# Performance work log

Hardware: AMD Instinct MI355X
Metric: run time of the kernel (lower is better)

Reference implementation:

```python
import jax, jax.numpy as jnp
import numpy as np

EMBED = 128   # embed_dim
HEADS = 8
POINTS = 4
H_SP, W_SP = 51, 102   # hardcoded spatial_shapes in __init__
BEV = 100              # bev_res
HRES = 50              # height_res


def _make_ref_points():
    """Exact numpy replica of the spherical grid built in __init__."""
    eps = 1e-6
    x = np.linspace(-71 / 2, 71 / 2, BEV)
    y = np.linspace(-71 / 2, 71 / 2, BEV)
    z = np.linspace(-50 / 2, 50 / 2, HRES)
    gx, gy, gz = np.meshgrid(x, y, z, indexing='ij')
    phi = np.sign(gy + eps) * np.arccos(gx / (np.sqrt(gx ** 2 + gy ** 2) + eps))
    theta = np.arccos(gz / (np.sqrt(gx ** 2 + gy ** 2 + gz ** 2) + eps))
    phi = 2 * np.pi - phi
    phi[phi > 2 * np.pi] -= 2 * np.pi
    col = phi / (2 * np.pi)   # grd_col_cross
    row = theta / np.pi       # grd_row_cross
    ref = np.stack([col, row], axis=-1)              # (BEV, BEV, HRES, 2)
    ref = ref.transpose(2, 0, 1, 3).reshape(HRES, BEV * BEV, 2)
    return jnp.asarray(ref, dtype=jnp.float32)


def setup_inputs() -> dict:
    key = jax.random.key(0)
    ks = jax.random.split(key, 12)
    d = EMBED
    s = 0.02
    return {
        'query': jax.random.normal(ks[0], (1, BEV * BEV, d), jnp.float32),
        'value': jax.random.normal(ks[1], (1, H_SP * W_SP, d), jnp.float32),
        'ref_points': _make_ref_points(),
        'W_off': jax.random.normal(ks[2], (d, HEADS * POINTS * 2), jnp.float32) * s,
        'b_off': jax.random.normal(ks[3], (HEADS * POINTS * 2,), jnp.float32) * s,
        'W_attn': jax.random.normal(ks[4], (d, HEADS * POINTS), jnp.float32) * s,
        'b_attn': jax.random.normal(ks[5], (HEADS * POINTS,), jnp.float32) * s,
        'W_val': jax.random.normal(ks[6], (d, d), jnp.float32) * s,
        'b_val': jax.random.normal(ks[7], (d,), jnp.float32) * s,
        'W_out': jax.random.normal(ks[8], (d, d), jnp.float32) * s,
        'b_out': jax.random.normal(ks[9], (d,), jnp.float32) * s,
        'W_proj': jax.random.normal(ks[10], (d, 1), jnp.float32) * s,
        'b_proj': jax.random.normal(ks[11], (1,), jnp.float32) * s,
    }


def _bilinear_sample(vflat, loc):
    """grid_sample(bilinear, zero padding, align_corners=False).
    vflat: (B, H*W, hd) value maps; loc: (B, N, 2) normalized [0,1] (x,y)."""
    px = loc[..., 0] * W_SP - 0.5
    py = loc[..., 1] * H_SP - 0.5
    x0 = jnp.floor(px)
    y0 = jnp.floor(py)
    dx = (px - x0)[..., None]
    dy = (py - y0)[..., None]
    x0i = x0.astype(jnp.int32)
    y0i = y0.astype(jnp.int32)

    def gather(xi, yi):
        valid = (xi >= 0) & (xi < W_SP) & (yi >= 0) & (yi < H_SP)
        idx = jnp.clip(yi, 0, H_SP - 1) * W_SP + jnp.clip(xi, 0, W_SP - 1)
        v = jnp.take_along_axis(vflat, idx[..., None], axis=1)  # (B, N, hd)
        return v * valid[..., None].astype(vflat.dtype)

    v00 = gather(x0i, y0i)
    v01 = gather(x0i + 1, y0i)
    v10 = gather(x0i, y0i + 1)
    v11 = gather(x0i + 1, y0i + 1)
    return (v00 * (1 - dx) * (1 - dy) + v01 * dx * (1 - dy)
            + v10 * (1 - dx) * dy + v11 * dx * dy)


def reference(query, value, ref_points, W_off, b_off, W_attn, b_attn,
              W_val, b_val, W_out, b_out, W_proj, b_proj):
    bs, nq, d = query.shape
    hd = d // HEADS
    L = ref_points.shape[0]

    # query-dependent MSDA projections (identical across height levels)
    offsets = (query @ W_off + b_off).reshape(bs, nq, HEADS, POINTS, 2)
    aw = jax.nn.softmax((query @ W_attn + b_attn).reshape(bs, nq, HEADS, POINTS), axis=-1)
    awt = aw.transpose(0, 2, 1, 3)                              # (bs, heads, nq, points)
    v = (value @ W_val + b_val).reshape(bs, -1, HEADS, hd)
    vflat = v.transpose(0, 2, 1, 3).reshape(bs * HEADS, H_SP * W_SP, hd)
    norm = jnp.asarray([W_SP, H_SP], dtype=query.dtype)         # offset_normalizer [W, H]

    def per_level(ref):  # ref: (nq, 2) -> MSDA output with its internal residual
        loc = ref[None, :, None, None, :] + offsets / norm      # (bs, nq, heads, pts, 2)
        loc = loc.transpose(0, 2, 1, 3, 4).reshape(bs * HEADS, nq * POINTS, 2)
        samp = _bilinear_sample(vflat, loc).reshape(bs, HEADS, nq, POINTS, hd)
        out = jnp.einsum('bhnp,bhnpd->bnhd', awt, samp).reshape(bs, nq, d)
        return out @ W_out + b_out + query                      # mmcv MSDA adds identity

    grd = jax.vmap(per_level)(ref_points)                       # (L, bs, nq, d)
    grd_3d = grd.transpose(1, 2, 0, 3).reshape(bs, BEV, BEV, L, d)
    weights = jax.nn.softmax(grd_3d @ W_proj + b_proj, axis=3)  # (bs, BEV, BEV, L, 1)
    max_height_index = jnp.argmax(weights, axis=3)              # (bs, BEV, BEV, 1)
    grd_bev = (weights * grd_3d).sum(axis=3)                    # (bs, BEV, BEV, d)
    return grd_bev.reshape(bs, nq, d) + query, max_height_index
```

## Files before the change

### kernel.cpp

```cpp
#include <hip/hip_runtime.h>
#include <math.h>

#define EMBED   128
#define NHEADS  8
#define NPOINTS 4
#define HD      16
#define HSP     51
#define WSP     102
#define NPIX    (HSP * WSP)
#define NQ      10000
#define NLVL    50

__global__ __launch_bounds__(128) void k_prep(
    const float* __restrict__ value,
    const float* __restrict__ Wv,
    const float* __restrict__ bv,
    const float* __restrict__ query,
    const float* __restrict__ Woff,
    const float* __restrict__ boff,
    const float* __restrict__ Wattn,
    const float* __restrict__ battn,
    const float* __restrict__ Wout,
    const float* __restrict__ Wproj,
    float* __restrict__ vout,
    float* __restrict__ off_out,
    float* __restrict__ aw_out,
    float* __restrict__ u_out) {
    const int b = blockIdx.x;
    const int t = threadIdx.x;

    if (b < NPIX) {
        __shared__ float vrow[EMBED];
        vrow[t] = value[(size_t)b * EMBED + t];
        __syncthreads();
        float acc = bv[t];
#pragma unroll 8
        for (int k = 0; k < EMBED; ++k)
            acc = fmaf(vrow[k], Wv[(size_t)k * EMBED + t], acc);
        const int h = t >> 4, c = t & 15;
        vout[((size_t)h * NPIX + b) * HD + c] = acc;
    } else if (b < NPIX + NQ) {
        const int q = b - NPIX;
        __shared__ float qrow[EMBED];
        __shared__ float attn[32];
        qrow[t] = query[(size_t)q * EMBED + t];
        __syncthreads();
        if (t < 64) {
            float acc = boff[t];
#pragma unroll 8
            for (int k = 0; k < EMBED; ++k)
                acc = fmaf(qrow[k], Woff[(size_t)k * 64 + t], acc);
            off_out[(size_t)q * 64 + t] = acc;
        } else if (t < 96) {
            const int j = t - 64;
            float acc = battn[j];
#pragma unroll 8
            for (int k = 0; k < EMBED; ++k)
                acc = fmaf(qrow[k], Wattn[(size_t)k * 32 + j], acc);
            attn[j] = acc;
        }
        __syncthreads();
        if (t < NHEADS) {
            const float a0 = attn[t * 4 + 0], a1 = attn[t * 4 + 1];
            const float a2 = attn[t * 4 + 2], a3 = attn[t * 4 + 3];
            const float mx = fmaxf(fmaxf(a0, a1), fmaxf(a2, a3));
            const float e0 = __expf(a0 - mx), e1 = __expf(a1 - mx);
            const float e2 = __expf(a2 - mx), e3 = __expf(a3 - mx);
            const float inv = 1.f / (e0 + e1 + e2 + e3);
            aw_out[(size_t)q * 32 + t * 4 + 0] = e0 * inv;
            aw_out[(size_t)q * 32 + t * 4 + 1] = e1 * inv;
            aw_out[(size_t)q * 32 + t * 4 + 2] = e2 * inv;
            aw_out[(size_t)q * 32 + t * 4 + 3] = e3 * inv;
        }
    } else {
        float acc = 0.f;
#pragma unroll 8
        for (int d = 0; d < EMBED; ++d)
            acc = fmaf(Wout[(size_t)t * EMBED + d], Wproj[d], acc);
        u_out[t] = acc;
    }
}

__global__ __launch_bounds__(256) void k_main(
    const float* __restrict__ query,
    const float* __restrict__ refp,
    const float* __restrict__ voff,
    const float* __restrict__ vaw,
    const float* __restrict__ vflat,
    const float* __restrict__ uvec,
    const float* __restrict__ Wout,
    const float* __restrict__ bout,
    float* __restrict__ out0,
    float* __restrict__ out1) {
    const int t = threadIdx.x;
    const int slot = t >> 6;
    const int lane = t & 63;
    const int half = lane >> 5;
    const int sub  = lane & 31;
    const int h  = sub >> 2;
    const int c4 = sub & 3;
    const int q = blockIdx.x * 4 + slot;

    __shared__ float s_rpy[4][NLVL];
    __shared__ float4 s_lds[4][32];

    {
        int i = t;
        if (i < 4 * NLVL) {
            const int ql = i / NLVL, l = i - ql * NLVL;
            const int qq = blockIdx.x * 4 + ql;
            s_rpy[ql][l] = refp[((size_t)l * NQ + qq) * 2 + 1];
        }
    }

    const float4* offp = (const float4*)(voff + (size_t)q * 64 + h * 8);
    const float4 o01 = offp[0];
    const float4 o23 = offp[1];
    const float4 awv4 = *(const float4*)(vaw + (size_t)q * 32 + h * 4);
    const float4 u4 = *(const float4*)(uvec + h * 16 + c4 * 4);
    const float rpx = refp[(size_t)q * 2];
    const float4* vbase = (const float4*)vflat + (size_t)h * NPIX * 4 + c4;

    const float offx[4] = {o01.x, o01.z, o23.x, o23.z};
    const float offy[4] = {o01.y, o01.w, o23.y, o23.w};
    const float awv[4]  = {awv4.x, awv4.y, awv4.z, awv4.w};

    float wx0[NPOINTS], wx1[NPOINTS], oyc[NPOINTS];
    int xo0[NPOINTS], xo1[NPOINTS];
#pragma unroll
    for (int p = 0; p < NPOINTS; ++p) {
        const float px = fmaf(rpx, (float)WSP, offx[p]) - 0.5f;
        const float fx = floorf(px);
        const float dx = px - fx;
        const int x0 = (int)fx, x1 = x0 + 1;
        const float a = awv[p];
        wx0[p] = ((unsigned)x0 < (unsigned)WSP) ? a * (1.f - dx) : 0.f;
        wx1[p] = ((unsigned)x1 < (unsigned)WSP) ? a * dx : 0.f;
        xo0[p] = min(max(x0, 0), WSP - 1) * 4;
        xo1[p] = min(max(x1, 0), WSP - 1) * 4;
        oyc[p] = offy[p] - 0.5f;
    }

    __syncthreads();

    float4 acc = {0.f, 0.f, 0.f, 0.f};
    float Z = 0.f, m = -1e30f;
    int best = 0;

#pragma unroll 2
    for (int i = 0; i < NLVL / 2; ++i) {
        const int l = 2 * i + half;
        const float rpy = s_rpy[slot][l];
        float4 s = {0.f, 0.f, 0.f, 0.f};
#pragma unroll
        for (int p = 0; p < NPOINTS; ++p) {
            const float py = fmaf(rpy, (float)HSP, oyc[p]);
            const float fy = floorf(py);
            const float dy = py - fy;
            const int y0 = (int)fy, y1 = y0 + 1;
            const float t0 = ((unsigned)y0 < (unsigned)HSP) ? (1.f - dy) : 0.f;
            const float t1 = ((unsigned)y1 < (unsigned)HSP) ? dy : 0.f;
            const int rb0 = min(max(y0, 0), HSP - 1) * (WSP * 4);
            const int rb1 = min(max(y1, 0), HSP - 1) * (WSP * 4);
            const float w00 = wx0[p] * t0;
            const float w01 = wx1[p] * t0;
            const float w10 = wx0[p] * t1;
            const float w11 = wx1[p] * t1;
            const float4 v00 = vbase[rb0 + xo0[p]];
            const float4 v01 = vbase[rb0 + xo1[p]];
            const float4 v10 = vbase[rb1 + xo0[p]];
            const float4 v11 = vbase[rb1 + xo1[p]];
            s.x = fmaf(w00, v00.x, s.x); s.y = fmaf(w00, v00.y, s.y);
            s.z = fmaf(w00, v00.z, s.z); s.w = fmaf(w00, v00.w, s.w);
            s.x = fmaf(w01, v01.x, s.x); s.y = fmaf(w01, v01.y, s.y);
            s.z = fmaf(w01, v01.z, s.z); s.w = fmaf(w01, v01.w, s.w);
            s.x = fmaf(w10, v10.x, s.x); s.y = fmaf(w10, v10.y, s.y);
            s.z = fmaf(w10, v10.z, s.z); s.w = fmaf(w10, v10.w, s.w);
            s.x = fmaf(w11, v11.x, s.x); s.y = fmaf(w11, v11.y, s.y);
            s.z = fmaf(w11, v11.z, s.z); s.w = fmaf(w11, v11.w, s.w);
        }
        float part = s.x * u4.x;
        part = fmaf(s.y, u4.y, part);
        part = fmaf(s.z, u4.z, part);
        part = fmaf(s.w, u4.w, part);
#pragma unroll
        for (int d = 1; d < 32; d <<= 1)
            part += __shfl_xor(part, d, 64);
        const float e = __expf(part);
        Z += e;
        acc.x = fmaf(e, s.x, acc.x);
        acc.y = fmaf(e, s.y, acc.y);
        acc.z = fmaf(e, s.z, acc.z);
        acc.w = fmaf(e, s.w, acc.w);
        best = (part > m) ? l : best;
        m = fmaxf(part, m);
    }

    {
        const float mo = __shfl_xor(m, 32, 64);
        const int   bo = __shfl_xor(best, 32, 64);
        const float Zo = __shfl_xor(Z, 32, 64);
        const float ax = __shfl_xor(acc.x, 32, 64);
        const float ay = __shfl_xor(acc.y, 32, 64);
        const float az = __shfl_xor(acc.z, 32, 64);
        const float aw_ = __shfl_xor(acc.w, 32, 64);
        const bool takeOther = (mo > m) || (mo == m && bo < best);
        best = takeOther ? bo : best;
        Z += Zo;
        acc.x += ax; acc.y += ay; acc.z += az; acc.w += aw_;
    }
    const float inv = 1.f / Z;
    if (half == 0) {
        float4 sv;
        sv.x = acc.x * inv; sv.y = acc.y * inv;
        sv.z = acc.z * inv; sv.w = acc.w * inv;
        s_lds[slot][sub] = sv;
        if (sub == 0) out1[q] = (float)best;
    }
    __syncthreads();

    const int dpb = sub * 4;
    float4 r = {0.f, 0.f, 0.f, 0.f};
    if (half == 0) {
        const float4 b4 = *(const float4*)(bout + dpb);
        const float4 q4 = *(const float4*)(query + (size_t)q * EMBED + dpb);
        r.x = fmaf(2.f, q4.x, b4.x);
        r.y = fmaf(2.f, q4.y, b4.y);
        r.z = fmaf(2.f, q4.z, b4.z);
        r.w = fmaf(2.f, q4.w, b4.w);
    }
    const float4* srow = s_lds[slot];
    const int cg0 = half * 16;
#pragma unroll 4
    for (int cg = cg0; cg < cg0 + 16; ++cg) {
        const float4 s4 = srow[cg];
        const float4 w0 = *(const float4*)(Wout + (size_t)(cg * 4 + 0) * EMBED + dpb);
        const float4 w1 = *(const float4*)(Wout + (size_t)(cg * 4 + 1) * EMBED + dpb);
        const float4 w2 = *(const float4*)(Wout + (size_t)(cg * 4 + 2) * EMBED + dpb);
        const float4 w3 = *(const float4*)(Wout + (size_t)(cg * 4 + 3) * EMBED + dpb);
        r.x = fmaf(s4.x, w0.x, r.x); r.y = fmaf(s4.x, w0.y, r.y);
        r.z = fmaf(s4.x, w0.z, r.z); r.w = fmaf(s4.x, w0.w, r.w);
        r.x = fmaf(s4.y, w1.x, r.x); r.y = fmaf(s4.y, w1.y, r.y);
        r.z = fmaf(s4.y, w1.z, r.z); r.w = fmaf(s4.y, w1.w, r.w);
        r.x = fmaf(s4.z, w2.x, r.x); r.y = fmaf(s4.z, w2.y, r.y);
        r.z = fmaf(s4.z, w2.z, r.z); r.w = fmaf(s4.z, w2.w, r.w);
        r.x = fmaf(s4.w, w3.x, r.x); r.y = fmaf(s4.w, w3.y, r.y);
        r.z = fmaf(s4.w, w3.z, r.z); r.w = fmaf(s4.w, w3.w, r.w);
    }
    {
        const float rx = __shfl_xor(r.x, 32, 64);
        const float ry = __shfl_xor(r.y, 32, 64);
        const float rz = __shfl_xor(r.z, 32, 64);
        const float rw = __shfl_xor(r.w, 32, 64);
        r.x += rx; r.y += ry; r.z += rz; r.w += rw;
    }
    if (half == 0)
        *(float4*)(out0 + (size_t)q * EMBED + dpb) = r;
}

extern "C" void kernel_launch(void* const* d_in, const int* in_sizes, int n_in,
                              void* d_out, int out_size, void* d_ws, size_t ws_size,
                              hipStream_t stream) {
    const float* query = (const float*)d_in[0];
    const float* value = (const float*)d_in[1];
    const float* refp  = (const float*)d_in[2];
    const float* Woff  = (const float*)d_in[3];
    const float* boff  = (const float*)d_in[4];
    const float* Wattn = (const float*)d_in[5];
    const float* battn = (const float*)d_in[6];
    const float* Wval  = (const float*)d_in[7];
    const float* bval  = (const float*)d_in[8];
    const float* Wout  = (const float*)d_in[9];
    const float* bout  = (const float*)d_in[10];
    const float* Wproj = (const float*)d_in[11];

    float* ws = (float*)d_ws;
    float* ws_v   = ws;
    float* ws_off = ws_v + (size_t)NHEADS * NPIX * HD;
    float* ws_aw  = ws_off + (size_t)NQ * 64;
    float* ws_u   = ws_aw + (size_t)NQ * 32;

    float* out0 = (float*)d_out;
    float* out1 = out0 + (size_t)NQ * EMBED;

    hipLaunchKernelGGL(k_prep, dim3(NPIX + NQ + 1), dim3(128), 0, stream,
                       value, Wval, bval, query, Woff, boff, Wattn, battn,
                       Wout, Wproj, ws_v, ws_off, ws_aw, ws_u);
    hipLaunchKernelGGL(k_main, dim3(NQ / 4), dim3(256), 0, stream,
                       query, refp, ws_off, ws_aw, ws_v, ws_u, Wout, bout,
                       out0, out1);
}
```

Baseline: 253.6 us.

## Split level loop across two waves per query and pack two rows per prep block

```diff
diff --git a/kernel.cpp b/kernel.cpp
--- a/kernel.cpp
+++ b/kernel.cpp
@@ -11,7 +11,10 @@
 #define NQ      10000
 #define NLVL    50
 
-__global__ __launch_bounds__(128) void k_prep(
+#define NPB_A ((NPIX + 1) / 2)
+#define NPB_B (NQ / 2)
+
+__global__ __launch_bounds__(256) void k_prep(
     const float* __restrict__ value,
     const float* __restrict__ Wv,
     const float* __restrict__ bv,
@@ -28,60 +31,67 @@
     float* __restrict__ u_out) {
     const int b = blockIdx.x;
     const int t = threadIdx.x;
-
-    if (b < NPIX) {
-        __shared__ float vrow[EMBED];
-        vrow[t] = value[(size_t)b * EMBED + t];
+    const int unit = t >> 7;
+    const int tt = t & 127;
+
+    if (b < NPB_A) {
+        __shared__ float vrow[2][EMBED];
+        const int pix = b * 2 + unit;
+        vrow[unit][tt] = value[(size_t)pix * EMBED + tt];
         __syncthreads();
-        float acc = bv[t];
+        float acc = bv[tt];
+        const float* vr = vrow[unit];
 #pragma unroll 8
         for (int k = 0; k < EMBED; ++k)
-            acc = fmaf(vrow[k], Wv[(size_t)k * EMBED + t], acc);
-        const int h = t >> 4, c = t & 15;
-        vout[((size_t)h * NPIX + b) * HD + c] = acc;
-    } else if (b < NPIX + NQ) {
-        const int q = b - NPIX;
-        __shared__ float qrow[EMBED];
-        __shared__ float attn[32];
-        qrow[t] = query[(size_t)q * EMBED + t];
+            acc = fmaf(vr[k], Wv[(size_t)k * EMBED + tt], acc);
+        const int h = tt >> 4, c = tt & 15;
+        vout[((size_t)h * NPIX + pix) * HD + c] = acc;
+    } else if (b < NPB_A + NPB_B) {
+        const int q = (b - NPB_A) * 2 + unit;
+        __shared__ float qrow[2][EMBED];
+        __shared__ float attn[2][32];
+        qrow[unit][tt] = query[(size_t)q * EMBED + tt];
         __syncthreads();
-        if (t < 64) {
-            float acc = boff[t];
+        const float* qr = qrow[unit];
+        if (tt < 64) {
+            float acc = boff[tt];
 #pragma unroll 8
             for (int k = 0; k < EMBED; ++k)
-                acc = fmaf(qrow[k], Woff[(size_t)k * 64 + t], acc);
-            off_out[(size_t)q * 64 + t] = acc;
-        } else if (t < 96) {
-            const int j = t - 64;
+                acc = fmaf(qr[k], Woff[(size_t)k * 64 + tt], acc);
+            off_out[(size_t)q * 64 + tt] = acc;
+        } else if (tt < 96) {
+            const int j = tt - 64;
             float acc = battn[j];
 #pragma unroll 8
             for (int k = 0; k < EMBED; ++k)
-                acc = fmaf(qrow[k], Wattn[(size_t)k * 32 + j], acc);
-            attn[j] = acc;
+                acc = fmaf(qr[k], Wattn[(size_t)k * 32 + j], acc);
+            attn[unit][j] = acc;
         }
         __syncthreads();
-        if (t < NHEADS) {
-            const float a0 = attn[t * 4 + 0], a1 = attn[t * 4 + 1];
-            const float a2 = attn[t * 4 + 2], a3 = attn[t * 4 + 3];
+        if (tt < NHEADS) {
+            const float a0 = attn[unit][tt * 4 + 0], a1 = attn[unit][tt * 4 + 1];
+            const float a2 = attn[unit][tt * 4 + 2], a3 = attn[unit][tt * 4 + 3];
             const float mx = fmaxf(fmaxf(a0, a1), fmaxf(a2, a3));
             const float e0 = __expf(a0 - mx), e1 = __expf(a1 - mx);
             const float e2 = __expf(a2 - mx), e3 = __expf(a3 - mx);
             const float inv = 1.f / (e0 + e1 + e2 + e3);
-            aw_out[(size_t)q * 32 + t * 4 + 0] = e0 * inv;
-            aw_out[(size_t)q * 32 + t * 4 + 1] = e1 * inv;
-            aw_out[(size_t)q * 32 + t * 4 + 2] = e2 * inv;
-            aw_out[(size_t)q * 32 + t * 4 + 3] = e3 * inv;
+            aw_out[(size_t)q * 32 + tt * 4 + 0] = e0 * inv;
+            aw_out[(size_t)q * 32 + tt * 4 + 1] = e1 * inv;
+            aw_out[(size_t)q * 32 + tt * 4 + 2] = e2 * inv;
+            aw_out[(size_t)q * 32 + tt * 4 + 3] = e3 * inv;
         }
     } else {
-        float acc = 0.f;
+        if (unit == 0) {
+            float acc = 0.f;
 #pragma unroll 8
-        for (int d = 0; d < EMBED; ++d)
-            acc = fmaf(Wout[(size_t)t * EMBED + d], Wproj[d], acc);
-        u_out[t] = acc;
+            for (int d = 0; d < EMBED; ++d)
+                acc = fmaf(Wout[(size_t)tt * EMBED + d], Wproj[d], acc);
+            u_out[tt] = acc;
+        }
     }
 }
 
-__global__ __launch_bounds__(256) void k_main(
+__global__ __launch_bounds__(256, 6) void k_main(
     const float* __restrict__ query,
     const float* __restrict__ refp,
     const float* __restrict__ voff,
@@ -93,24 +103,23 @@
     float* __restrict__ out0,
     float* __restrict__ out1) {
     const int t = threadIdx.x;
-    const int slot = t >> 6;
-    const int lane = t & 63;
-    const int half = lane >> 5;
-    const int sub  = lane & 31;
+    const int qslot = t >> 7;
+    const int w2 = (t >> 6) & 1;
+    const int half = (t >> 5) & 1;
+    const int sub = t & 31;
     const int h  = sub >> 2;
     const int c4 = sub & 3;
-    const int q = blockIdx.x * 4 + slot;
-
-    __shared__ float s_rpy[4][NLVL];
-    __shared__ float4 s_lds[4][32];
-
-    {
-        int i = t;
-        if (i < 4 * NLVL) {
-            const int ql = i / NLVL, l = i - ql * NLVL;
-            const int qq = blockIdx.x * 4 + ql;
-            s_rpy[ql][l] = refp[((size_t)l * NQ + qq) * 2 + 1];
-        }
+    const int q = blockIdx.x * 2 + qslot;
+
+    __shared__ float  s_rpy[2][NLVL];
+    __shared__ float4 s_acc[2][32];
+    __shared__ float  s_z[2], s_m[2];
+    __shared__ int    s_b[2];
+
+    if (t < 2 * NLVL) {
+        const int ql = t / NLVL, l = t - ql * NLVL;
+        const int qq = blockIdx.x * 2 + ql;
+        s_rpy[ql][l] = refp[((size_t)l * NQ + qq) * 2 + 1];
     }
 
     const float4* offp = (const float4*)(voff + (size_t)q * 64 + h * 8);
@@ -147,10 +156,11 @@
     float Z = 0.f, m = -1e30f;
     int best = 0;
 
-#pragma unroll 2
-    for (int i = 0; i < NLVL / 2; ++i) {
-        const int l = 2 * i + half;
-        const float rpy = s_rpy[slot][l];
+#pragma unroll 1
+    for (int i = 0; i < 13; ++i) {
+        if (4 * i + (w2 << 1) >= NLVL) break;
+        const int l = 4 * i + (w2 << 1) + half;
+        const float rpy = s_rpy[qslot][l];
         float4 s = {0.f, 0.f, 0.f, 0.f};
 #pragma unroll
         for (int p = 0; p < NPOINTS; ++p) {
@@ -206,56 +216,74 @@
         const float aw_ = __shfl_xor(acc.w, 32, 64);
         const bool takeOther = (mo > m) || (mo == m && bo < best);
         best = takeOther ? bo : best;
+        m = fmaxf(m, mo);
         Z += Zo;
         acc.x += ax; acc.y += ay; acc.z += az; acc.w += aw_;
     }
-    const float inv = 1.f / Z;
-    if (half == 0) {
-        float4 sv;
-        sv.x = acc.x * inv; sv.y = acc.y * inv;
-        sv.z = acc.z * inv; sv.w = acc.w * inv;
-        s_lds[slot][sub] = sv;
-        if (sub == 0) out1[q] = (float)best;
+
+    if (w2 == 1) {
+        if (half == 0) s_acc[qslot][sub] = acc;
+        if ((t & 63) == 0) { s_z[qslot] = Z; s_m[qslot] = m; s_b[qslot] = best; }
     }
     __syncthreads();
 
-    const int dpb = sub * 4;
-    float4 r = {0.f, 0.f, 0.f, 0.f};
-    if (half == 0) {
-        const float4 b4 = *(const float4*)(bout + dpb);
-        const float4 q4 = *(const float4*)(query + (size_t)q * EMBED + dpb);
-        r.x = fmaf(2.f, q4.x, b4.x);
-        r.y = fmaf(2.f, q4.y, b4.y);
-        r.z = fmaf(2.f, q4.z, b4.z);
-        r.w = fmaf(2.f, q4.w, b4.w);
-    }
-    const float4* srow = s_lds[slot];
-    const int cg0 = half * 16;
+    if (w2 == 0) {
+        const float4 ao = s_acc[qslot][sub];
+        const float Zo = s_z[qslot];
+        const float mo = s_m[qslot];
+        const int   bo = s_b[qslot];
+        const bool takeOther = (mo > m) || (mo == m && bo < best);
+        best = takeOther ? bo : best;
+        Z += Zo;
+        acc.x += ao.x; acc.y += ao.y; acc.z += ao.z; acc.w += ao.w;
+
+        const float inv = 1.f / Z;
+        if (half == 0) {
+            float4 sv;
+            sv.x = acc.x * inv; sv.y = acc.y * inv;
+            sv.z = acc.z * inv; sv.w = acc.w * inv;
+            s_acc[qslot][sub] = sv;
+            if (sub == 0) out1[q] = (float)best;
+        }
+
+        const int dpb = sub * 4;
+        float4 r = {0.f, 0.f, 0.f, 0.f};
+        if (half == 0) {
+            const float4 b4 = *(const float4*)(bout + dpb);
+            const float4 q4 = *(const float4*)(query + (size_t)q * EMBED + dpb);
+            r.x = fmaf(2.f, q4.x, b4.x);
+            r.y = fmaf(2.f, q4.y, b4.y);
+            r.z = fmaf(2.f, q4.z, b4.z);
+            r.w = fmaf(2.f, q4.w, b4.w);
+        }
+        const float4* srow = s_acc[qslot];
+        const int cg0 = half * 16;
 #pragma unroll 4
-    for (int cg = cg0; cg < cg0 + 16; ++cg) {
-        const float4 s4 = srow[cg];
-        const float4 w0 = *(const float4*)(Wout + (size_t)(cg * 4 + 0) * EMBED + dpb);
-        const float4 w1 = *(const float4*)(Wout + (size_t)(cg * 4 + 1) * EMBED + dpb);
-        const float4 w2 = *(const float4*)(Wout + (size_t)(cg * 4 + 2) * EMBED + dpb);
-        const float4 w3 = *(const float4*)(Wout + (size_t)(cg * 4 + 3) * EMBED + dpb);
-        r.x = fmaf(s4.x, w0.x, r.x); r.y = fmaf(s4.x, w0.y, r.y);
-        r.z = fmaf(s4.x, w0.z, r.z); r.w = fmaf(s4.x, w0.w, r.w);
-        r.x = fmaf(s4.y, w1.x, r.x); r.y = fmaf(s4.y, w1.y, r.y);
-        r.z = fmaf(s4.y, w1.z, r.z); r.w = fmaf(s4.y, w1.w, r.w);
-        r.x = fmaf(s4.z, w2.x, r.x); r.y = fmaf(s4.z, w2.y, r.y);
-        r.z = fmaf(s4.z, w2.z, r.z); r.w = fmaf(s4.z, w2.w, r.w);
-        r.x = fmaf(s4.w, w3.x, r.x); r.y = fmaf(s4.w, w3.y, r.y);
-        r.z = fmaf(s4.w, w3.z, r.z); r.w = fmaf(s4.w, w3.w, r.w);
-    }
-    {
-        const float rx = __shfl_xor(r.x, 32, 64);
-        const float ry = __shfl_xor(r.y, 32, 64);
-        const float rz = __shfl_xor(r.z, 32, 64);
-        const float rw = __shfl_xor(r.w, 32, 64);
-        r.x += rx; r.y += ry; r.z += rz; r.w += rw;
-    }
-    if (half == 0)
-        *(float4*)(out0 + (size_t)q * EMBED + dpb) = r;
+        for (int cg = cg0; cg < cg0 + 16; ++cg) {
+            const float4 s4 = srow[cg];
+            const float4 w0 = *(const float4*)(Wout + (size_t)(cg * 4 + 0) * EMBED + dpb);
+            const float4 w1 = *(const float4*)(Wout + (size_t)(cg * 4 + 1) * EMBED + dpb);
+            const float4 w2v = *(const float4*)(Wout + (size_t)(cg * 4 + 2) * EMBED + dpb);
+            const float4 w3 = *(const float4*)(Wout + (size_t)(cg * 4 + 3) * EMBED + dpb);
+            r.x = fmaf(s4.x, w0.x, r.x); r.y = fmaf(s4.x, w0.y, r.y);
+            r.z = fmaf(s4.x, w0.z, r.z); r.w = fmaf(s4.x, w0.w, r.w);
+            r.x = fmaf(s4.y, w1.x, r.x); r.y = fmaf(s4.y, w1.y, r.y);
+            r.z = fmaf(s4.y, w1.z, r.z); r.w = fmaf(s4.y, w1.w, r.w);
+            r.x = fmaf(s4.z, w2v.x, r.x); r.y = fmaf(s4.z, w2v.y, r.y);
+            r.z = fmaf(s4.z, w2v.z, r.z); r.w = fmaf(s4.z, w2v.w, r.w);
+            r.x = fmaf(s4.w, w3.x, r.x); r.y = fmaf(s4.w, w3.y, r.y);
+            r.z = fmaf(s4.w, w3.z, r.z); r.w = fmaf(s4.w, w3.w, r.w);
+        }
+        {
+            const float rx = __shfl_xor(r.x, 32, 64);
+            const float ry = __shfl_xor(r.y, 32, 64);
+            const float rz = __shfl_xor(r.z, 32, 64);
+            const float rw = __shfl_xor(r.w, 32, 64);
+            r.x += rx; r.y += ry; r.z += rz; r.w += rw;
+        }
+        if (half == 0)
+            *(float4*)(out0 + (size_t)q * EMBED + dpb) = r;
+    }
 }
 
 extern "C" void kernel_launch(void* const* d_in, const int* in_sizes, int n_in,
@@ -283,10 +311,10 @@
     float* out0 = (float*)d_out;
     float* out1 = out0 + (size_t)NQ * EMBED;
 
-    hipLaunchKernelGGL(k_prep, dim3(NPIX + NQ + 1), dim3(128), 0, stream,
+    hipLaunchKernelGGL(k_prep, dim3(NPB_A + NPB_B + 1), dim3(256), 0, stream,
                        value, Wval, bval, query, Woff, boff, Wattn, battn,
                        Wout, Wproj, ws_v, ws_off, ws_aw, ws_u);
-    hipLaunchKernelGGL(k_main, dim3(NQ / 4), dim3(256), 0, stream,
+    hipLaunchKernelGGL(k_main, dim3(NQ / 2), dim3(256), 0, stream,
                        query, refp, ws_off, ws_aw, ws_v, ws_u, Wout, bout,
                        out0, out1);
 }
```

Result: no change. 253.1 us (-0.2%).
